# Kernel optimization log

Hardware: AMD Instinct MI355X
Metric: run time of the kernel (lower is better)

The kernel has to match this reference:

```python
import jax, jax.numpy as jnp
import numpy as np

MS = (1, 2, 4, 8, 16, 32)  # ms_token_size; last entry == H == W
A = -0.75  # PyTorch bicubic coefficient


def _cubic_w(t, a=A):
    t = abs(float(t))
    if t <= 1.0:
        return (a + 2.0) * t**3 - (a + 3.0) * t**2 + 1.0
    if t < 2.0:
        return a * t**3 - 5.0 * a * t**2 + 8.0 * a * t - 4.0 * a
    return 0.0


def _bicubic_matrix(n_in, n_out):
    # Dense [n_out, n_in] matrix reproducing F.interpolate(mode='bicubic',
    # align_corners=False) with border-clamped taps (PyTorch semantics).
    M = np.zeros((n_out, n_in), np.float32)
    s = n_in / n_out
    for i in range(n_out):
        x = (i + 0.5) * s - 0.5
        x0 = int(np.floor(x))
        t = x - x0
        for off in (-1, 0, 1, 2):
            j = min(max(x0 + off, 0), n_in - 1)
            M[i, j] += _cubic_w(off - t)
    return jnp.asarray(M)


def _area_down(x, pn):
    # 'area' interpolation with integer factor == average pooling
    B, C, H, W = x.shape
    f = H // pn
    return x.reshape(B, C, pn, f, pn, f).mean(axis=(3, 5))


def _bicubic_up(x, Mh, Mw):
    # separable bicubic: y = Mh @ x @ Mw^T per (b, c)
    return jnp.einsum('hi,wj,bcij->bchw', Mh, Mw, x)


def setup_inputs() -> dict:
    key = jax.random.key(0)
    k1, k2 = jax.random.split(key)
    z_enc = jax.random.normal(k1, (16, 128, 32, 32), dtype=jnp.float32)
    emb = jax.random.normal(k2, (8192, 128), dtype=jnp.float32) * 1.0  # std=1.0
    return {"z_enc": z_enc, "emb": emb}


def reference(z_enc, emb):
    B, C, H, W = z_enc.shape
    n_levels = len(MS)
    # z_enc is detached in the original (z_enc.detach())
    z_rest = jax.lax.stop_gradient(z_enc)
    z_dec = jnp.zeros_like(z_rest)
    e_sq = jnp.sum(emb * emb, axis=1)  # [V]
    ret = []
    for step, pn in enumerate(MS):
        last = step == n_levels - 1
        zd = z_rest if last else _area_down(z_rest, pn)
        flat = zd.transpose(0, 2, 3, 1).reshape(-1, C)  # [B*pn*pn, C]
        # ||z||^2 + ||e||^2 - 2 z e^T
        dist = jnp.sum(flat * flat, axis=1, keepdims=True) + e_sq \
               - 2.0 * (flat @ emb.T)
        token = jnp.argmin(dist, axis=1)  # [B*pn*pn]
        zq = emb[token].reshape(B, pn, pn, C).transpose(0, 3, 1, 2)  # [B,C,pn,pn]
        if last:
            zu = zq
        else:
            Mh = _bicubic_matrix(pn, H)
            Mw = _bicubic_matrix(pn, W)
            zu = _bicubic_up(zq, Mh, Mw)
        z_dec = z_dec + zu
        z_rest = z_rest - zu
        ret.append(z_dec)
    return jnp.stack(ret)  # [n_levels, B, C, H, W]
```

## Files before the change

### kernel.cpp

```cpp
#include <hip/hip_runtime.h>
#include <hip/hip_bf16.h>

#define NCODES 8192
#define CDIM 128
#define NTOT (16*128*32*32)
#define KTOT 22272

typedef __attribute__((ext_vector_type(8))) short bf16x8;
typedef __attribute__((ext_vector_type(16))) float f32x16;
typedef unsigned long long u64;
typedef unsigned int u32;
typedef unsigned short ushort_t;

__device__ __forceinline__ ushort_t f2bf(float x) {
    u32 u = __float_as_uint(x);
    u32 r = (u + 0x7FFFu + ((u >> 16) & 1u)) >> 16;
    return (ushort_t)r;
}
__device__ __forceinline__ float bf2f(ushort_t h) {
    return __uint_as_float(((u32)h) << 16);
}

__device__ __forceinline__ void gload_lds16(const void* g, void* l) {
    __builtin_amdgcn_global_load_lds(
        (const __attribute__((address_space(1))) unsigned int*)g,
        (__attribute__((address_space(3))) unsigned int*)l, 16, 0, 0);
}

__global__ __launch_bounds__(256) void pack_emb_kernel(const float* __restrict__ src,
        ushort_t* __restrict__ dst, float* __restrict__ esq) {
    __shared__ float sm[32][129];
    int rb = blockIdx.x, t = threadIdx.x;
    int rl = t >> 3, d0 = (t & 7) * 16;
    const float4* s4 = (const float4*)(src + (size_t)(rb * 32 + rl) * CDIM + d0);
    #pragma unroll
    for (int j = 0; j < 4; j++) {
        float4 v = s4[j];
        sm[rl][d0 + 4*j + 0] = v.x; sm[rl][d0 + 4*j + 1] = v.y;
        sm[rl][d0 + 4*j + 2] = v.z; sm[rl][d0 + 4*j + 3] = v.w;
    }
    __syncthreads();
    {
        int r = t >> 3, g = t & 7;
        float s = 0.f;
        #pragma unroll
        for (int k = 0; k < 16; k++) { float x = sm[r][g * 16 + k]; s += x * x; }
        s += __shfl_xor(s, 1, 64);
        s += __shfl_xor(s, 2, 64);
        s += __shfl_xor(s, 4, 64);
        if (g == 0) esq[rb * 32 + r] = s;
    }
    #pragma unroll
    for (int k = 0; k < 2; k++) {
        int s = t + 256 * k;
        int c = s >> 6, l = s & 63;
        int r = l & 31, dbase = c * 16 + (l >> 5) * 8;
        bf16x8 vh, vl;
        #pragma unroll
        for (int e = 0; e < 8; e++) {
            float x = sm[r][dbase + e];
            ushort_t hh = f2bf(x);
            vh[e] = (short)hh;
            vl[e] = (short)f2bf(x - bf2f(hh));
        }
        size_t base = ((size_t)(rb * 8 + c) * 2) * 512 + (size_t)l * 8;
        *(bf16x8*)(dst + base)       = vh;
        *(bf16x8*)(dst + base + 512) = vl;
    }
}

__global__ __launch_bounds__(256) void down_kernel(const float* __restrict__ src,
        float* __restrict__ zd, u64* __restrict__ keys) {
    int gi = blockIdx.x * 256 + threadIdx.x;
    if (gi < KTOT) keys[gi] = ~0ull;
    int t    = gi;
    int item = t >> 6;
    int wi   = t & 63;
    int row = item >> 7, dim = item & 127;
    const float* sp = src + (((size_t)row * CDIM + dim) * 32) * 32;
    float s = 0.f;
    #pragma unroll
    for (int k = 0; k < 16; k++) {
        int flat = wi * 16 + k;
        s += sp[(flat >> 5) * 32 + (flat & 31)];
    }
    #pragma unroll
    for (int d = 32; d; d >>= 1) s += __shfl_xor(s, d, 64);
    if (wi == 0) zd[(size_t)row * CDIM + dim] = s * (1.0f / 1024.0f);
}

__global__ __launch_bounds__(512) void argmin_kernel(
        const float* __restrict__ zsrc, const ushort_t* __restrict__ bpk,
        const float* __restrict__ esq, u64* __restrict__ keys,
        int tiles, int slices, int nrows, int bchw) {
    __shared__ ushort_t lds[2][16384];
    __shared__ float es_lds[2048];

    int cps = NCODES / slices;
    int steps = cps >> 6;
    int bid = blockIdx.x;
    int tile  = bid / slices;
    int slice = bid % slices;
    int code0 = slice * cps;
    int tid = threadIdx.x, wv = tid >> 6, l = tid & 63, l31 = l & 31, lh = l >> 5;

    int rb = tile * 8 + wv;
    bf16x8 a_h[8], a_l[8];
    if (bchw) {
        int b = rb >> 5, h = rb & 31;
        const float* zr = zsrc + (size_t)b * 131072 + h * 32 + l31;
        #pragma unroll
        for (int c = 0; c < 8; c++) {
            #pragma unroll
            for (int e = 0; e < 8; e++) {
                int d = c * 16 + lh * 8 + e;
                float x = -2.0f * zr[(size_t)d * 1024];
                ushort_t hh = f2bf(x);
                a_h[c][e] = (short)hh;
                a_l[c][e] = (short)f2bf(x - bf2f(hh));
            }
        }
    } else {
        int row = rb * 32 + l31;
        if (row > nrows - 1) row = nrows - 1;
        const float* zr = zsrc + (size_t)row * CDIM + lh * 8;
        #pragma unroll
        for (int c = 0; c < 8; c++) {
            float4 f0 = *(const float4*)(zr + c * 16);
            float4 f1 = *(const float4*)(zr + c * 16 + 4);
            float xs[8] = {f0.x, f0.y, f0.z, f0.w, f1.x, f1.y, f1.z, f1.w};
            #pragma unroll
            for (int e = 0; e < 8; e++) {
                float x = -2.0f * xs[e];
                ushort_t hh = f2bf(x);
                a_h[c][e] = (short)hh;
                a_l[c][e] = (short)f2bf(x - bf2f(hh));
            }
        }
    }
    float ev0 = 0.f, ev1 = 0.f, ev2 = 0.f, ev3 = 0.f;
    if (tid < cps)        ev0 = esq[code0 + tid];
    if (512  + tid < cps) ev1 = esq[code0 + 512 + tid];
    if (1024 + tid < cps) ev2 = esq[code0 + 1024 + tid];
    if (1536 + tid < cps) ev3 = esq[code0 + 1536 + tid];
    __builtin_amdgcn_sched_barrier(0);

    const char* bbase = (const char*)bpk + (size_t)(code0 >> 6) * 32768;
    {
        const char* g0 = bbase + (size_t)wv * 4096 + (size_t)l * 16;
        ushort_t* d0 = &lds[0][wv * 2048];
        gload_lds16(g0,        d0);
        gload_lds16(g0 + 1024, d0 + 512);
        gload_lds16(g0 + 2048, d0 + 1024);
        gload_lds16(g0 + 3072, d0 + 1536);
    }
    __builtin_amdgcn_sched_barrier(0);
    if (tid < cps)        es_lds[tid] = ev0;
    if (512  + tid < cps) es_lds[512 + tid] = ev1;
    if (1024 + tid < cps) es_lds[1024 + tid] = ev2;
    if (1536 + tid < cps) es_lds[1536 + tid] = ev3;
    asm volatile("s_waitcnt lgkmcnt(0)" ::: "memory");

    float best[16];
    int   bidx[16];
    #pragma unroll
    for (int r = 0; r < 16; r++) { best[r] = 1e38f; bidx[r] = 0; }

    for (int t = 0; t < steps; ++t) {
        asm volatile("s_waitcnt vmcnt(0)" ::: "memory");
        __builtin_amdgcn_s_barrier();
        if (t + 1 < steps) {
            const char* g = bbase + (size_t)(t + 1) * 32768
                          + (size_t)wv * 4096 + (size_t)l * 16;
            ushort_t* d = &lds[(t + 1) & 1][wv * 2048];
            gload_lds16(g,        d);
            gload_lds16(g + 1024, d + 512);
            gload_lds16(g + 2048, d + 1024);
            gload_lds16(g + 3072, d + 1536);
        }
        float es0 = es_lds[(t << 6) + l31];
        float es1 = es_lds[(t << 6) + 32 + l31];
        f32x16 acc0, acc1;
        #pragma unroll
        for (int r = 0; r < 16; r++) { acc0[r] = es0; acc1[r] = es1; }
        const ushort_t* lp = &lds[t & 1][0] + l * 8;
        __builtin_amdgcn_s_setprio(1);
        #pragma unroll
        for (int c = 0; c < 8; c++) {
            bf16x8 g0h = *(const bf16x8*)(lp + (2 * c) * 512);
            bf16x8 g0l = *(const bf16x8*)(lp + (2 * c + 1) * 512);
            bf16x8 g1h = *(const bf16x8*)(lp + 8192 + (2 * c) * 512);
            bf16x8 g1l = *(const bf16x8*)(lp + 8192 + (2 * c + 1) * 512);
            acc0 = __builtin_amdgcn_mfma_f32_32x32x16_bf16(a_h[c], g0h, acc0, 0, 0, 0);
            acc1 = __builtin_amdgcn_mfma_f32_32x32x16_bf16(a_h[c], g1h, acc1, 0, 0, 0);
            acc0 = __builtin_amdgcn_mfma_f32_32x32x16_bf16(a_h[c], g0l, acc0, 0, 0, 0);
            acc1 = __builtin_amdgcn_mfma_f32_32x32x16_bf16(a_h[c], g1l, acc1, 0, 0, 0);
            acc0 = __builtin_amdgcn_mfma_f32_32x32x16_bf16(a_l[c], g0h, acc0, 0, 0, 0);
            acc1 = __builtin_amdgcn_mfma_f32_32x32x16_bf16(a_l[c], g1h, acc1, 0, 0, 0);
        }
        __builtin_amdgcn_s_setprio(0);
        int code = code0 + (t << 6) + l31;
        #pragma unroll
        for (int r = 0; r < 16; r++) {
            float s0 = acc0[r], s1 = acc1[r];
            float m  = fminf(s0, s1);
            int   ci = (s0 <= s1) ? code : code + 32;
            bool lt = m < best[r];
            best[r] = lt ? m : best[r];
            bidx[r] = lt ? ci : bidx[r];
        }
    }

    #pragma unroll
    for (int r = 0; r < 16; r++) {
        u32 fb = __float_as_uint(best[r]);
        fb = (fb & 0x80000000u) ? ~fb : (fb | 0x80000000u);
        u64 key = ((u64)fb << 32) | (u32)bidx[r];
        #pragma unroll
        for (int d = 1; d < 32; d <<= 1) {
            u64 o = __shfl_xor(key, d, 64);
            key = (o < key) ? o : key;
        }
        if (l31 == 0) {
            int rw = tile * 256 + wv * 32 + (r & 3) + 8 * (r >> 2) + 4 * lh;
            atomicMin(&keys[rw], key);
        }
    }
}

__device__ __forceinline__ float cubicw(float t) {
    float t2 = t * t;
    if (t <= 1.0f) return (1.25f * t - 2.25f) * t2 + 1.0f;
    return -0.75f * (((t - 5.0f) * t + 8.0f) * t - 4.0f);
}

__global__ __launch_bounds__(256) void up_kernel(
        const float* __restrict__ emb,
        const u64* __restrict__ keys,
        const float* __restrict__ src,
        const float* __restrict__ prev,
        float* __restrict__ zrest,
        float* __restrict__ out,
        float* __restrict__ zd_next,
        int pn, int last, int first, int pnn) {
    __shared__ float wtab[32][4];
    __shared__ int   itab[32][4];
    __shared__ float smp[512];
    int tid = threadIdx.x;
    if (!last && tid < 128) {
        int pos = tid >> 2, tap = tid & 3;
        float s  = (float)pn * (1.0f / 32.0f);
        float x  = ((float)pos + 0.5f) * s - 0.5f;
        float x0 = floorf(x);
        float t  = x - x0;
        int   off = tap - 1;
        float w  = cubicw(fabsf((float)off - t));
        int   jj = (int)x0 + off;
        jj = min(max(jj, 0), pn - 1);
        wtab[pos][tap] = w;
        itab[pos][tap] = jj;
    }
    __syncthreads();

    int t  = blockIdx.x * 256 + tid;
    int w4 = (t & 7) << 2;
    int h  = (t >> 3) & 31;
    int c  = (t >> 8) & 127;
    int b  = t >> 15;
    size_t i = (((size_t)b * CDIM + c) * 32 + h) * 32 + w4;

    float zu[4];
    if (last) {
        int kb = (b << 10) + (h << 5) + w4;
        #pragma unroll
        for (int j = 0; j < 4; j++) {
            int tok = (int)(keys[kb + j] & 0xFFFFFFFFull);
            zu[j] = emb[(size_t)tok * CDIM + c];
        }
    } else {
        int base = b * pn * pn;
        #pragma unroll
        for (int j = 0; j < 4; j++) zu[j] = 0.f;
        #pragma unroll
        for (int u = 0; u < 4; u++) {
            float whu = wtab[h][u];
            int   ih  = itab[h][u] * pn;
            #pragma unroll
            for (int j = 0; j < 4; j++) {
                float acc = 0.f;
                #pragma unroll
                for (int v = 0; v < 4; v++) {
                    int tok = (int)(keys[base + ih + itab[w4 + j][v]] & 0xFFFFFFFFull);
                    acc += wtab[w4 + j][v] * emb[(size_t)tok * CDIM + c];
                }
                zu[j] += whu * acc;
            }
        }
    }
    float4 sv = *(const float4*)(src + i);
    float4 pv = {0.f, 0.f, 0.f, 0.f};
    if (!first) pv = *(const float4*)(prev + i);
    float4 ov, rv;
    ov.x = pv.x + zu[0]; ov.y = pv.y + zu[1]; ov.z = pv.z + zu[2]; ov.w = pv.w + zu[3];
    rv.x = sv.x - zu[0]; rv.y = sv.y - zu[1]; rv.z = sv.z - zu[2]; rv.w = sv.w - zu[3];
    *(float4*)(out + i)   = ov;
    *(float4*)(zrest + i) = rv;

    if (pnn) {
        int f = 32 / pnn;
        if (f >= 4) {
            smp[h * 8 + (w4 >> 2)] = (rv.x + rv.y) + (rv.z + rv.w);
        } else {
            smp[h * 16 + (w4 >> 1)]     = rv.x + rv.y;
            smp[h * 16 + (w4 >> 1) + 1] = rv.z + rv.w;
        }
        __syncthreads();
        int W = pnn * pnn;
        if (tid < W) {
            int lb = __builtin_ctz(pnn);
            int ph = tid >> lb, pw = tid & (pnn - 1);
            float s = 0.f;
            if (f >= 4) {
                int cg = f >> 2;
                for (int u = 0; u < f; u++)
                    for (int v = 0; v < cg; v++)
                        s += smp[(ph * f + u) * 8 + pw * cg + v];
            } else {
                s = smp[(2 * ph) * 16 + pw] + smp[(2 * ph + 1) * 16 + pw];
            }
            int b2 = blockIdx.x >> 7, c2 = blockIdx.x & 127;
            int row = (b2 * pnn + ph) * pnn + pw;
            zd_next[(size_t)row * CDIM + c2] = s * (1.0f / (float)(f * f));
        }
    }
}

extern "C" void kernel_launch(void* const* d_in, const int* in_sizes, int n_in,
                              void* d_out, int out_size, void* d_ws, size_t ws_size,
                              hipStream_t stream) {
    const float* z_enc = (const float*)d_in[0];
    const float* emb   = (const float*)d_in[1];
    float* out = (float*)d_out;
    float* ws  = (float*)d_ws;

    float*    zrest  = ws;
    float*    zd_f32 = ws + 2097152;
    ushort_t* emb_pk = (ushort_t*)(ws + 4194304);
    float*    esq    = ws + 5242880;
    u64*      keys   = (u64*)(ws + 5251072);

    pack_emb_kernel<<<NCODES / 32, 256, 0, stream>>>(emb, emb_pk, esq);
    down_kernel<<<512, 256, 0, stream>>>(z_enc, zd_f32, keys);

    const int MS_[6]   = {1, 2, 4, 8, 16, 32};
    const int SL_[6]   = {128, 128, 128, 64, 16, 4};
    const int KOFF_[6] = {0, 256, 512, 768, 1792, 5888};
    for (int lvl = 0; lvl < 6; lvl++) {
        int pn     = MS_[lvl];
        int rows   = 16 * pn * pn;
        int tiles  = (rows + 255) / 256;
        int slices = SL_[lvl];
        const float* src = lvl ? zrest : z_enc;

        argmin_kernel<<<tiles * slices, 512, 0, stream>>>(
            lvl == 5 ? zrest : zd_f32, emb_pk, esq, keys + KOFF_[lvl],
            tiles, slices, rows, lvl == 5 ? 1 : 0);
        int pnn = (lvl < 4) ? MS_[lvl + 1] : 0;
        up_kernel<<<NTOT / 4 / 256, 256, 0, stream>>>(
            emb, keys + KOFF_[lvl], src, lvl ? (out + (size_t)(lvl - 1) * NTOT) : out,
            zrest, out + (size_t)lvl * NTOT, zd_f32,
            pn, lvl == 5 ? 1 : 0, lvl == 0 ? 1 : 0, pnn);
    }
}
```

Measured before the change: 418.3 us.

## Process two row tiles per wave so each codebook LDS fragment is reused

Each wave now keeps A-operand fragments for two 32-row blocks and loops over the two 32-code halves, so every codebook fragment read from LDS feeds two row tiles instead of one. A block therefore covers 512 rows instead of 256. Slice counts and key offsets are rescaled so the grid sizes stay comparable. This halves LDS codebook traffic per MFMA, at the cost of doubling the best/index registers and the A-fragment registers, which raises register pressure and may lower occupancy.

```diff
diff --git a/kernel.cpp b/kernel.cpp
--- a/kernel.cpp
+++ b/kernel.cpp
@@ -4,7 +4,7 @@
 #define NCODES 8192
 #define CDIM 128
 #define NTOT (16*128*32*32)
-#define KTOT 22272
+#define KTOT 23040
 
 typedef __attribute__((ext_vector_type(8))) short bf16x8;
 typedef __attribute__((ext_vector_type(16))) float f32x16;
@@ -94,7 +94,7 @@
         const float* __restrict__ esq, u64* __restrict__ keys,
         int tiles, int slices, int nrows, int bchw) {
     __shared__ ushort_t lds[2][16384];
-    __shared__ float es_lds[2048];
+    __shared__ float es_lds[1024];
 
     int cps = NCODES / slices;
     int steps = cps >> 6;
@@ -104,45 +104,47 @@
     int code0 = slice * cps;
     int tid = threadIdx.x, wv = tid >> 6, l = tid & 63, l31 = l & 31, lh = l >> 5;
 
-    int rb = tile * 8 + wv;
-    bf16x8 a_h[8], a_l[8];
-    if (bchw) {
-        int b = rb >> 5, h = rb & 31;
-        const float* zr = zsrc + (size_t)b * 131072 + h * 32 + l31;
-        #pragma unroll
-        for (int c = 0; c < 8; c++) {
-            #pragma unroll
-            for (int e = 0; e < 8; e++) {
-                int d = c * 16 + lh * 8 + e;
-                float x = -2.0f * zr[(size_t)d * 1024];
-                ushort_t hh = f2bf(x);
-                a_h[c][e] = (short)hh;
-                a_l[c][e] = (short)f2bf(x - bf2f(hh));
-            }
-        }
-    } else {
-        int row = rb * 32 + l31;
-        if (row > nrows - 1) row = nrows - 1;
-        const float* zr = zsrc + (size_t)row * CDIM + lh * 8;
-        #pragma unroll
-        for (int c = 0; c < 8; c++) {
-            float4 f0 = *(const float4*)(zr + c * 16);
-            float4 f1 = *(const float4*)(zr + c * 16 + 4);
-            float xs[8] = {f0.x, f0.y, f0.z, f0.w, f1.x, f1.y, f1.z, f1.w};
-            #pragma unroll
-            for (int e = 0; e < 8; e++) {
-                float x = -2.0f * xs[e];
-                ushort_t hh = f2bf(x);
-                a_h[c][e] = (short)hh;
-                a_l[c][e] = (short)f2bf(x - bf2f(hh));
-            }
-        }
-    }
-    float ev0 = 0.f, ev1 = 0.f, ev2 = 0.f, ev3 = 0.f;
-    if (tid < cps)        ev0 = esq[code0 + tid];
-    if (512  + tid < cps) ev1 = esq[code0 + 512 + tid];
-    if (1024 + tid < cps) ev2 = esq[code0 + 1024 + tid];
-    if (1536 + tid < cps) ev3 = esq[code0 + 1536 + tid];
+    int rb0 = tile * 16 + wv * 2;
+    bf16x8 t0h[8], t0l[8], t1h[8], t1l[8];
+    #pragma unroll
+    for (int rt = 0; rt < 2; rt++) {
+        int rb = rb0 + rt;
+        if (bchw) {
+            int b = rb >> 5, h = rb & 31;
+            const float* zr = zsrc + (size_t)b * 131072 + h * 32 + l31;
+            #pragma unroll
+            for (int c = 0; c < 8; c++) {
+                #pragma unroll
+                for (int e = 0; e < 8; e++) {
+                    int d = c * 16 + lh * 8 + e;
+                    float x = -2.0f * zr[(size_t)d * 1024];
+                    ushort_t hh = f2bf(x);
+                    if (rt) { t1h[c][e] = (short)hh; t1l[c][e] = (short)f2bf(x - bf2f(hh)); }
+                    else    { t0h[c][e] = (short)hh; t0l[c][e] = (short)f2bf(x - bf2f(hh)); }
+                }
+            }
+        } else {
+            int row = rb * 32 + l31;
+            if (row > nrows - 1) row = nrows - 1;
+            const float* zr = zsrc + (size_t)row * CDIM + lh * 8;
+            #pragma unroll
+            for (int c = 0; c < 8; c++) {
+                float4 f0 = *(const float4*)(zr + c * 16);
+                float4 f1 = *(const float4*)(zr + c * 16 + 4);
+                float xs[8] = {f0.x, f0.y, f0.z, f0.w, f1.x, f1.y, f1.z, f1.w};
+                #pragma unroll
+                for (int e = 0; e < 8; e++) {
+                    float x = -2.0f * xs[e];
+                    ushort_t hh = f2bf(x);
+                    if (rt) { t1h[c][e] = (short)hh; t1l[c][e] = (short)f2bf(x - bf2f(hh)); }
+                    else    { t0h[c][e] = (short)hh; t0l[c][e] = (short)f2bf(x - bf2f(hh)); }
+                }
+            }
+        }
+    }
+    float ev0 = 0.f, ev1 = 0.f;
+    if (tid < cps)       ev0 = esq[code0 + tid];
+    if (512 + tid < cps) ev1 = esq[code0 + 512 + tid];
     __builtin_amdgcn_sched_barrier(0);
 
     const char* bbase = (const char*)bpk + (size_t)(code0 >> 6) * 32768;
@@ -155,16 +157,14 @@
         gload_lds16(g0 + 3072, d0 + 1536);
     }
     __builtin_amdgcn_sched_barrier(0);
-    if (tid < cps)        es_lds[tid] = ev0;
-    if (512  + tid < cps) es_lds[512 + tid] = ev1;
-    if (1024 + tid < cps) es_lds[1024 + tid] = ev2;
-    if (1536 + tid < cps) es_lds[1536 + tid] = ev3;
+    if (tid < cps)       es_lds[tid] = ev0;
+    if (512 + tid < cps) es_lds[512 + tid] = ev1;
     asm volatile("s_waitcnt lgkmcnt(0)" ::: "memory");
 
-    float best[16];
-    int   bidx[16];
-    #pragma unroll
-    for (int r = 0; r < 16; r++) { best[r] = 1e38f; bidx[r] = 0; }
+    float best[32];
+    int   bidx[32];
+    #pragma unroll
+    for (int r = 0; r < 32; r++) { best[r] = 1e38f; bidx[r] = 0; }
 
     for (int t = 0; t < steps; ++t) {
         asm volatile("s_waitcnt vmcnt(0)" ::: "memory");
@@ -178,52 +178,59 @@
             gload_lds16(g + 2048, d + 1024);
             gload_lds16(g + 3072, d + 1536);
         }
-        float es0 = es_lds[(t << 6) + l31];
-        float es1 = es_lds[(t << 6) + 32 + l31];
-        f32x16 acc0, acc1;
-        #pragma unroll
-        for (int r = 0; r < 16; r++) { acc0[r] = es0; acc1[r] = es1; }
-        const ushort_t* lp = &lds[t & 1][0] + l * 8;
+        const ushort_t* lpb = &lds[t & 1][0] + l * 8;
         __builtin_amdgcn_s_setprio(1);
         #pragma unroll
-        for (int c = 0; c < 8; c++) {
-            bf16x8 g0h = *(const bf16x8*)(lp + (2 * c) * 512);
-            bf16x8 g0l = *(const bf16x8*)(lp + (2 * c + 1) * 512);
-            bf16x8 g1h = *(const bf16x8*)(lp + 8192 + (2 * c) * 512);
-            bf16x8 g1l = *(const bf16x8*)(lp + 8192 + (2 * c + 1) * 512);
-            acc0 = __builtin_amdgcn_mfma_f32_32x32x16_bf16(a_h[c], g0h, acc0, 0, 0, 0);
-            acc1 = __builtin_amdgcn_mfma_f32_32x32x16_bf16(a_h[c], g1h, acc1, 0, 0, 0);
-            acc0 = __builtin_amdgcn_mfma_f32_32x32x16_bf16(a_h[c], g0l, acc0, 0, 0, 0);
-            acc1 = __builtin_amdgcn_mfma_f32_32x32x16_bf16(a_h[c], g1l, acc1, 0, 0, 0);
-            acc0 = __builtin_amdgcn_mfma_f32_32x32x16_bf16(a_l[c], g0h, acc0, 0, 0, 0);
-            acc1 = __builtin_amdgcn_mfma_f32_32x32x16_bf16(a_l[c], g1h, acc1, 0, 0, 0);
+        for (int g = 0; g < 2; g++) {
+            float es = es_lds[(t << 6) + (g << 5) + l31];
+            f32x16 acc0, acc1;
+            #pragma unroll
+            for (int r = 0; r < 16; r++) { acc0[r] = es; acc1[r] = es; }
+            const ushort_t* lp = lpb + g * 8192;
+            #pragma unroll
+            for (int c = 0; c < 8; c++) {
+                bf16x8 gh = *(const bf16x8*)(lp + (2 * c) * 512);
+                bf16x8 gl = *(const bf16x8*)(lp + (2 * c + 1) * 512);
+                acc0 = __builtin_amdgcn_mfma_f32_32x32x16_bf16(t0h[c], gh, acc0, 0, 0, 0);
+                acc1 = __builtin_amdgcn_mfma_f32_32x32x16_bf16(t1h[c], gh, acc1, 0, 0, 0);
+                acc0 = __builtin_amdgcn_mfma_f32_32x32x16_bf16(t0h[c], gl, acc0, 0, 0, 0);
+                acc1 = __builtin_amdgcn_mfma_f32_32x32x16_bf16(t1h[c], gl, acc1, 0, 0, 0);
+                acc0 = __builtin_amdgcn_mfma_f32_32x32x16_bf16(t0l[c], gh, acc0, 0, 0, 0);
+                acc1 = __builtin_amdgcn_mfma_f32_32x32x16_bf16(t1l[c], gh, acc1, 0, 0, 0);
+            }
+            int code = code0 + (t << 6) + (g << 5) + l31;
+            #pragma unroll
+            for (int r = 0; r < 16; r++) {
+                float s0 = acc0[r];
+                bool lt0 = s0 < best[r];
+                best[r] = lt0 ? s0 : best[r];
+                bidx[r] = lt0 ? code : bidx[r];
+                float s1 = acc1[r];
+                bool lt1 = s1 < best[16 + r];
+                best[16 + r] = lt1 ? s1 : best[16 + r];
+                bidx[16 + r] = lt1 ? code : bidx[16 + r];
+            }
         }
         __builtin_amdgcn_s_setprio(0);
-        int code = code0 + (t << 6) + l31;
+    }
+
+    #pragma unroll
+    for (int rt = 0; rt < 2; rt++) {
         #pragma unroll
         for (int r = 0; r < 16; r++) {
-            float s0 = acc0[r], s1 = acc1[r];
-            float m  = fminf(s0, s1);
-            int   ci = (s0 <= s1) ? code : code + 32;
-            bool lt = m < best[r];
-            best[r] = lt ? m : best[r];
-            bidx[r] = lt ? ci : bidx[r];
-        }
-    }
-
-    #pragma unroll
-    for (int r = 0; r < 16; r++) {
-        u32 fb = __float_as_uint(best[r]);
-        fb = (fb & 0x80000000u) ? ~fb : (fb | 0x80000000u);
-        u64 key = ((u64)fb << 32) | (u32)bidx[r];
-        #pragma unroll
-        for (int d = 1; d < 32; d <<= 1) {
-            u64 o = __shfl_xor(key, d, 64);
-            key = (o < key) ? o : key;
-        }
-        if (l31 == 0) {
-            int rw = tile * 256 + wv * 32 + (r & 3) + 8 * (r >> 2) + 4 * lh;
-            atomicMin(&keys[rw], key);
+            u32 fb = __float_as_uint(best[rt * 16 + r]);
+            fb = (fb & 0x80000000u) ? ~fb : (fb | 0x80000000u);
+            u64 key = ((u64)fb << 32) | (u32)bidx[rt * 16 + r];
+            #pragma unroll
+            for (int d = 1; d < 32; d <<= 1) {
+                u64 o = __shfl_xor(key, d, 64);
+                key = (o < key) ? o : key;
+            }
+            if (l31 == 0) {
+                int rw = tile * 512 + wv * 64 + rt * 32
+                       + (r & 3) + 8 * (r >> 2) + 4 * lh;
+                atomicMin(&keys[rw], key);
+            }
         }
     }
 }
@@ -353,12 +360,12 @@
     down_kernel<<<512, 256, 0, stream>>>(z_enc, zd_f32, keys);
 
     const int MS_[6]   = {1, 2, 4, 8, 16, 32};
-    const int SL_[6]   = {128, 128, 128, 64, 16, 4};
-    const int KOFF_[6] = {0, 256, 512, 768, 1792, 5888};
+    const int SL_[6]   = {128, 128, 128, 128, 32, 8};
+    const int KOFF_[6] = {0, 512, 1024, 1536, 2560, 6656};
     for (int lvl = 0; lvl < 6; lvl++) {
         int pn     = MS_[lvl];
         int rows   = 16 * pn * pn;
-        int tiles  = (rows + 255) / 256;
+        int tiles  = (rows + 511) / 512;
         int slices = SL_[lvl];
         const float* src = lvl ? zrest : z_enc;
 
```

After: 614.5 us. +46.9%, slower.

## Add 64-row argmin kernel with pre-packed split-bf16 activations for large levels

Applied to the files above, without the earlier changes.

For the two largest levels, activations are first packed into split hi/lo bf16 MFMA layout by dedicated pack kernels, including a transposing pack for the BCHW level. A new argmin kernel then has each wave handle 64 rows instead of 32, so every codebook fragment read from LDS feeds twice as many MFMAs. The slice count for these levels is doubled to keep the grid size up. The cost is two extra small kernel launches, twice the accumulator and best-index registers, which may lower occupancy, and more workspace.

```diff
diff --git a/kernel.cpp b/kernel.cpp
--- a/kernel.cpp
+++ b/kernel.cpp
@@ -64,6 +64,68 @@
             vl[e] = (short)f2bf(x - bf2f(hh));
         }
         size_t base = ((size_t)(rb * 8 + c) * 2) * 512 + (size_t)l * 8;
+        *(bf16x8*)(dst + base)       = vh;
+        *(bf16x8*)(dst + base + 512) = vl;
+    }
+}
+
+__global__ __launch_bounds__(256) void pack_kernel(const float* __restrict__ src,
+        ushort_t* __restrict__ dst) {
+    __shared__ float sm[32][129];
+    int rb = blockIdx.x, t = threadIdx.x;
+    int rl = t >> 3, d0 = (t & 7) * 16;
+    const float4* s4 = (const float4*)(src + (size_t)(rb * 32 + rl) * CDIM + d0);
+    #pragma unroll
+    for (int j = 0; j < 4; j++) {
+        float4 v = s4[j];
+        sm[rl][d0 + 4*j + 0] = v.x; sm[rl][d0 + 4*j + 1] = v.y;
+        sm[rl][d0 + 4*j + 2] = v.z; sm[rl][d0 + 4*j + 3] = v.w;
+    }
+    __syncthreads();
+    #pragma unroll
+    for (int k = 0; k < 2; k++) {
+        int s = t + 256 * k;
+        int c = s >> 6, l = s & 63;
+        int r = l & 31, dbase = c * 16 + (l >> 5) * 8;
+        bf16x8 vh, vl;
+        #pragma unroll
+        for (int e = 0; e < 8; e++) {
+            float x = sm[r][dbase + e] * -2.0f;
+            ushort_t hh = f2bf(x);
+            vh[e] = (short)hh;
+            vl[e] = (short)f2bf(x - bf2f(hh));
+        }
+        size_t base = ((size_t)(rb * 8 + c) * 2) * 512 + (size_t)l * 8;
+        *(bf16x8*)(dst + base)       = vh;
+        *(bf16x8*)(dst + base + 512) = vl;
+    }
+}
+
+__global__ __launch_bounds__(256) void pack_l5_kernel(const float* __restrict__ src,
+        ushort_t* __restrict__ dst) {
+    __shared__ float sm[128][36];
+    int bh = blockIdx.x;
+    int b = bh >> 5, h = bh & 31;
+    int t = threadIdx.x;
+    int d = t >> 1, w0 = (t & 1) * 16;
+    const float* sp = src + (((size_t)b * CDIM + d) * 32 + h) * 32 + w0;
+    #pragma unroll
+    for (int j = 0; j < 16; j++) sm[d][w0 + j] = sp[j];
+    __syncthreads();
+    #pragma unroll
+    for (int k = 0; k < 2; k++) {
+        int s = t + 256 * k;
+        int c = s >> 6, l = s & 63;
+        int w = l & 31, dbase = c * 16 + (l >> 5) * 8;
+        bf16x8 vh, vl;
+        #pragma unroll
+        for (int e = 0; e < 8; e++) {
+            float x = sm[dbase + e][w] * -2.0f;
+            ushort_t hh = f2bf(x);
+            vh[e] = (short)hh;
+            vl[e] = (short)f2bf(x - bf2f(hh));
+        }
+        size_t base = ((size_t)(bh * 8 + c) * 2) * 512 + (size_t)l * 8;
         *(bf16x8*)(dst + base)       = vh;
         *(bf16x8*)(dst + base + 512) = vl;
     }
@@ -92,7 +154,7 @@
 __global__ __launch_bounds__(512) void argmin_kernel(
         const float* __restrict__ zsrc, const ushort_t* __restrict__ bpk,
         const float* __restrict__ esq, u64* __restrict__ keys,
-        int tiles, int slices, int nrows, int bchw) {
+        int tiles, int slices, int nrows) {
     __shared__ ushort_t lds[2][16384];
     __shared__ float es_lds[2048];
 
@@ -106,21 +168,7 @@
 
     int rb = tile * 8 + wv;
     bf16x8 a_h[8], a_l[8];
-    if (bchw) {
-        int b = rb >> 5, h = rb & 31;
-        const float* zr = zsrc + (size_t)b * 131072 + h * 32 + l31;
-        #pragma unroll
-        for (int c = 0; c < 8; c++) {
-            #pragma unroll
-            for (int e = 0; e < 8; e++) {
-                int d = c * 16 + lh * 8 + e;
-                float x = -2.0f * zr[(size_t)d * 1024];
-                ushort_t hh = f2bf(x);
-                a_h[c][e] = (short)hh;
-                a_l[c][e] = (short)f2bf(x - bf2f(hh));
-            }
-        }
-    } else {
+    {
         int row = rb * 32 + l31;
         if (row > nrows - 1) row = nrows - 1;
         const float* zr = zsrc + (size_t)row * CDIM + lh * 8;
@@ -224,6 +272,124 @@
         if (l31 == 0) {
             int rw = tile * 256 + wv * 32 + (r & 3) + 8 * (r >> 2) + 4 * lh;
             atomicMin(&keys[rw], key);
+        }
+    }
+}
+
+__global__ __launch_bounds__(512) void argmin64_kernel(
+        const ushort_t* __restrict__ apk, const ushort_t* __restrict__ bpk,
+        const float* __restrict__ esq, u64* __restrict__ keys,
+        int tiles, int slices) {
+    __shared__ ushort_t lds[2][16384];
+    __shared__ float es_lds[1024];
+
+    int cps = NCODES / slices;
+    int steps = cps >> 6;
+    int bid = blockIdx.x;
+    int tile  = bid / slices;
+    int slice = bid % slices;
+    int code0 = slice * cps;
+    int tid = threadIdx.x, wv = tid >> 6, l = tid & 63, l31 = l & 31, lh = l >> 5;
+
+    int rb0 = tile * 16 + wv * 2;
+    const ushort_t* ap = apk + (size_t)rb0 * 8192 + l * 8;
+    bf16x8 a0h[8], a0l[8], a1h[8], a1l[8];
+    #pragma unroll
+    for (int c = 0; c < 8; c++) {
+        a0h[c] = *(const bf16x8*)(ap + (2 * c) * 512);
+        a0l[c] = *(const bf16x8*)(ap + (2 * c + 1) * 512);
+        a1h[c] = *(const bf16x8*)(ap + 8192 + (2 * c) * 512);
+        a1l[c] = *(const bf16x8*)(ap + 8192 + (2 * c + 1) * 512);
+    }
+    float ev0 = 0.f, ev1 = 0.f;
+    if (tid < cps)       ev0 = esq[code0 + tid];
+    if (512 + tid < cps) ev1 = esq[code0 + 512 + tid];
+    __builtin_amdgcn_sched_barrier(0);
+
+    const char* bbase = (const char*)bpk + (size_t)(code0 >> 6) * 32768;
+    {
+        const char* g0 = bbase + (size_t)wv * 4096 + (size_t)l * 16;
+        ushort_t* d0 = &lds[0][wv * 2048];
+        gload_lds16(g0,        d0);
+        gload_lds16(g0 + 1024, d0 + 512);
+        gload_lds16(g0 + 2048, d0 + 1024);
+        gload_lds16(g0 + 3072, d0 + 1536);
+    }
+    __builtin_amdgcn_sched_barrier(0);
+    if (tid < cps)       es_lds[tid] = ev0;
+    if (512 + tid < cps) es_lds[512 + tid] = ev1;
+    asm volatile("s_waitcnt lgkmcnt(0)" ::: "memory");
+
+    float best[32];
+    int   bidx[32];
+    #pragma unroll
+    for (int r = 0; r < 32; r++) { best[r] = 1e38f; bidx[r] = 0; }
+
+    for (int t = 0; t < steps; ++t) {
+        asm volatile("s_waitcnt vmcnt(0)" ::: "memory");
+        __builtin_amdgcn_s_barrier();
+        if (t + 1 < steps) {
+            const char* g = bbase + (size_t)(t + 1) * 32768
+                          + (size_t)wv * 4096 + (size_t)l * 16;
+            ushort_t* d = &lds[(t + 1) & 1][wv * 2048];
+            gload_lds16(g,        d);
+            gload_lds16(g + 1024, d + 512);
+            gload_lds16(g + 2048, d + 1024);
+            gload_lds16(g + 3072, d + 1536);
+        }
+        const ushort_t* lpb = &lds[t & 1][0] + l * 8;
+        __builtin_amdgcn_s_setprio(1);
+        #pragma unroll
+        for (int g = 0; g < 2; g++) {
+            float es = es_lds[(t << 6) + (g << 5) + l31];
+            f32x16 acc0, acc1;
+            #pragma unroll
+            for (int r = 0; r < 16; r++) { acc0[r] = es; acc1[r] = es; }
+            const ushort_t* lp = lpb + g * 8192;
+            #pragma unroll
+            for (int c = 0; c < 8; c++) {
+                bf16x8 gh = *(const bf16x8*)(lp + (2 * c) * 512);
+                bf16x8 gl = *(const bf16x8*)(lp + (2 * c + 1) * 512);
+                acc0 = __builtin_amdgcn_mfma_f32_32x32x16_bf16(a0h[c], gh, acc0, 0, 0, 0);
+                acc1 = __builtin_amdgcn_mfma_f32_32x32x16_bf16(a1h[c], gh, acc1, 0, 0, 0);
+                acc0 = __builtin_amdgcn_mfma_f32_32x32x16_bf16(a0h[c], gl, acc0, 0, 0, 0);
+                acc1 = __builtin_amdgcn_mfma_f32_32x32x16_bf16(a1h[c], gl, acc1, 0, 0, 0);
+                acc0 = __builtin_amdgcn_mfma_f32_32x32x16_bf16(a0l[c], gh, acc0, 0, 0, 0);
+                acc1 = __builtin_amdgcn_mfma_f32_32x32x16_bf16(a1l[c], gh, acc1, 0, 0, 0);
+            }
+            int code = code0 + (t << 6) + (g << 5) + l31;
+            #pragma unroll
+            for (int r = 0; r < 16; r++) {
+                float s0 = acc0[r];
+                bool lt0 = s0 < best[r];
+                best[r] = lt0 ? s0 : best[r];
+                bidx[r] = lt0 ? code : bidx[r];
+                float s1 = acc1[r];
+                bool lt1 = s1 < best[16 + r];
+                best[16 + r] = lt1 ? s1 : best[16 + r];
+                bidx[16 + r] = lt1 ? code : bidx[16 + r];
+            }
+        }
+        __builtin_amdgcn_s_setprio(0);
+    }
+
+    #pragma unroll
+    for (int rt = 0; rt < 2; rt++) {
+        #pragma unroll
+        for (int r = 0; r < 16; r++) {
+            u32 fb = __float_as_uint(best[rt * 16 + r]);
+            fb = (fb & 0x80000000u) ? ~fb : (fb | 0x80000000u);
+            u64 key = ((u64)fb << 32) | (u32)bidx[rt * 16 + r];
+            #pragma unroll
+            for (int d = 1; d < 32; d <<= 1) {
+                u64 o = __shfl_xor(key, d, 64);
+                key = (o < key) ? o : key;
+            }
+            if (l31 == 0) {
+                int rw = tile * 512 + wv * 64 + rt * 32
+                       + (r & 3) + 8 * (r >> 2) + 4 * lh;
+                atomicMin(&keys[rw], key);
+            }
         }
     }
 }
@@ -346,25 +512,33 @@
     float*    zrest  = ws;
     float*    zd_f32 = ws + 2097152;
     ushort_t* emb_pk = (ushort_t*)(ws + 4194304);
-    float*    esq    = ws + 5242880;
-    u64*      keys   = (u64*)(ws + 5251072);
+    ushort_t* zd_pk  = (ushort_t*)(ws + 5242880);
+    float*    esq    = ws + 7340032;
+    u64*      keys   = (u64*)(ws + 7348224);
 
     pack_emb_kernel<<<NCODES / 32, 256, 0, stream>>>(emb, emb_pk, esq);
     down_kernel<<<512, 256, 0, stream>>>(z_enc, zd_f32, keys);
 
     const int MS_[6]   = {1, 2, 4, 8, 16, 32};
-    const int SL_[6]   = {128, 128, 128, 64, 16, 4};
+    const int SL_[6]   = {128, 128, 128, 64, 32, 8};
     const int KOFF_[6] = {0, 256, 512, 768, 1792, 5888};
     for (int lvl = 0; lvl < 6; lvl++) {
         int pn     = MS_[lvl];
         int rows   = 16 * pn * pn;
-        int tiles  = (rows + 255) / 256;
         int slices = SL_[lvl];
         const float* src = lvl ? zrest : z_enc;
 
-        argmin_kernel<<<tiles * slices, 512, 0, stream>>>(
-            lvl == 5 ? zrest : zd_f32, emb_pk, esq, keys + KOFF_[lvl],
-            tiles, slices, rows, lvl == 5 ? 1 : 0);
+        if (lvl < 4) {
+            int tiles = (rows + 255) / 256;
+            argmin_kernel<<<tiles * slices, 512, 0, stream>>>(
+                zd_f32, emb_pk, esq, keys + KOFF_[lvl], tiles, slices, rows);
+        } else {
+            int tiles = rows / 512;
+            if (lvl == 4) pack_kernel<<<rows / 32, 256, 0, stream>>>(zd_f32, zd_pk);
+            else          pack_l5_kernel<<<512, 256, 0, stream>>>(zrest, zd_pk);
+            argmin64_kernel<<<tiles * slices, 512, 0, stream>>>(
+                zd_pk, emb_pk, esq, keys + KOFF_[lvl], tiles, slices);
+        }
         int pnn = (lvl < 4) ? MS_[lvl + 1] : 0;
         up_kernel<<<NTOT / 4 / 256, 256, 0, stream>>>(
             emb, keys + KOFF_[lvl], src, lvl ? (out + (size_t)(lvl - 1) * NTOT) : out,
```

New measurement: 434.4 us. 1.04x slower.
